# Performance work log

Hardware: AMD Instinct MI355X
Metric: run time of the kernel (lower is better)

## Reference

```python
import jax, jax.numpy as jnp
import numpy as np

B, N, F_IN = 64, 128, 128
H, MSG, L = 512, 512, 4
N_STEPS = 4
TARGET = 12
HIDDEN = (128, 256, 128)


def _mlp_params(key, n_in, n_out):
    dims = (n_in,) + HIDDEN + (n_out,)
    ps = []
    for i in range(len(dims) - 1):
        key, k1, k2 = jax.random.split(key, 3)
        s = 1.0 / np.sqrt(dims[i]).astype(np.float32)
        ps.append(jax.random.uniform(k1, (dims[i + 1], dims[i]), minval=-s, maxval=s, dtype=jnp.float32))
        ps.append(jax.random.uniform(k2, (dims[i + 1],), minval=-s, maxval=s, dtype=jnp.float32))
    return ps


def setup_inputs():
    key = jax.random.key(0)
    ks = jax.random.split(key, 10)
    g = (jax.random.uniform(ks[0], (B, N, N)) < 0.15).astype(jnp.float32)
    e = jax.random.randint(ks[1], (B, N, N), 0, L + 1).astype(jnp.float32) * g
    h_in = jax.random.normal(ks[2], (B, N, F_IN), dtype=jnp.float32)
    # trailing nodes are 'virtual' (zero features -> masked out by the model)
    node_on = (jnp.arange(N) < 112).astype(jnp.float32)
    h_in = h_in * node_on[None, :, None]
    g = g * node_on[None, :, None] * node_on[None, None, :]
    e = e * node_on[None, :, None] * node_on[None, None, :]
    A = jax.random.normal(ks[3], (L, H, MSG), dtype=jnp.float32)  # per-edge-label message matrices
    s = 1.0 / np.sqrt(H).astype(np.float32)
    gru_Wih = jax.random.uniform(ks[4], (3 * H, MSG), minval=-s, maxval=s, dtype=jnp.float32)
    gru_Whh = jax.random.uniform(ks[5], (3 * H, H), minval=-s, maxval=s, dtype=jnp.float32)
    gru_bih = jax.random.uniform(ks[6], (3 * H,), minval=-s, maxval=s, dtype=jnp.float32)
    gru_bhh = jax.random.uniform(ks[7], (3 * H,), minval=-s, maxval=s, dtype=jnp.float32)
    r1 = _mlp_params(ks[8], 2 * H, TARGET)
    r2 = _mlp_params(ks[9], H, TARGET)
    inp = dict(g=g, h_in=h_in, e=e, A=A, gru_Wih=gru_Wih, gru_Whh=gru_Whh,
               gru_bih=gru_bih, gru_bhh=gru_bhh)
    for i in range(4):
        inp['r1_W%d' % i], inp['r1_b%d' % i] = r1[2 * i], r1[2 * i + 1]
        inp['r2_W%d' % i], inp['r2_b%d' % i] = r2[2 * i], r2[2 * i + 1]
    return inp


def _mlp(x, Ws, bs):
    for W, b in zip(Ws[:-1], bs[:-1]):
        x = jax.nn.relu(x @ W.T + b)
    return x @ Ws[-1].T + bs[-1]


def _forward(g, h_in, e, A, gru_Wih, gru_Whh, gru_bih, gru_bhh, r1_Ws, r1_bs, r2_Ws, r2_bs):
    Bq, Nq, F = h_in.shape
    Lq, Hq, Mq = A.shape
    # zero-pad node features up to hidden size
    h0 = jnp.concatenate([h_in, jnp.zeros((Bq, Nq, Hq - F), h_in.dtype)], axis=-1)  # [B,N,H]
    node_mask = (jnp.sum(jnp.abs(h_in), axis=-1) > 0).astype(h_in.dtype)  # [B,N]
    labels = jnp.arange(1, Lq + 1, dtype=e.dtype)
    e_oh = (e[..., None] == labels).astype(h_in.dtype)  # [B,N,N,L] edge-label one-hot
    h = h0
    for _ in range(N_STEPS):
        # per-label projected states, then edge-conditioned masked-sum aggregation
        hproj = jnp.einsum('bwh,lhm->blwm', h, A)  # [B,L,N,MSG]
        m = jnp.einsum('bvwl,blwm,bvw->bvm', e_oh, hproj, g)  # [B,N,MSG]
        # one GRU step per node (vectorized), torch nn.GRU gate ordering r,z,n
        gi = m @ gru_Wih.T + gru_bih
        gh = h @ gru_Whh.T + gru_bhh
        i_r, i_z, i_n = jnp.split(gi, 3, axis=-1)
        h_r, h_z, h_n = jnp.split(gh, 3, axis=-1)
        r = jax.nn.sigmoid(i_r + h_r)
        z = jax.nn.sigmoid(i_z + h_z)
        n = jnp.tanh(i_n + r * h_n)
        h = ((1.0 - z) * n + z * h) * node_mask[..., None]
    # GGNN gated readout over nodes, masking virtual nodes
    gate = jax.nn.sigmoid(_mlp(jnp.concatenate([h, h0], axis=-1), r1_Ws, r1_bs))
    val = _mlp(h, r2_Ws, r2_bs)
    read_mask = (jnp.sum(h0, axis=-1) != 0).astype(h.dtype)  # [B,N]
    return jnp.sum(gate * val * read_mask[..., None], axis=1)  # [B,TARGET]


def reference(g, h_in, e, A, gru_Wih, gru_Whh, gru_bih, gru_bhh,
              r1_W0, r1_b0, r1_W1, r1_b1, r1_W2, r1_b2, r1_W3, r1_b3,
              r2_W0, r2_b0, r2_W1, r2_b1, r2_W2, r2_b2, r2_W3, r2_b3):
    return _forward(g, h_in, e, A, gru_Wih, gru_Whh, gru_bih, gru_bhh,
                    [r1_W0, r1_W1, r1_W2, r1_W3], [r1_b0, r1_b1, r1_b2, r1_b3],
                    [r2_W0, r2_W1, r2_W2, r2_W3], [r2_b0, r2_b1, r2_b2, r2_b3])
```

## Files before the change

### kernel.cpp

```cpp
#include <hip/hip_runtime.h>
#include <math.h>

#define B_     64
#define N_     128
#define FIN_   128
#define H_     512
#define MSG_   512
#define L_     4
#define NSTEPS_ 4
#define TGT_   12
#define ROWS_  (B_*N_)

typedef _Float16 f16;
typedef __attribute__((ext_vector_type(8))) _Float16 half8;
typedef __attribute__((ext_vector_type(4))) float f32x4;

__device__ inline void gload16(const void* g, void* l) {
    __builtin_amdgcn_global_load_lds((const __attribute__((address_space(1))) void*)g,
                                     (__attribute__((address_space(3))) void*)l,
                                     16, 0, 0);
}

__device__ inline void split_write(float v, f16* ph, f16* pl) {
    f16 hi = (f16)v;
    *ph = hi;
    *pl = (f16)(v - (float)hi);
}

__global__ void k_init(const float* __restrict__ h_in,
                       f16* __restrict__ hbh, f16* __restrict__ hbl,
                       float* __restrict__ nmask, float* __restrict__ rmask) {
    int bn = blockIdx.x;
    int t  = threadIdx.x;
    const float* src = h_in + (size_t)bn * FIN_;
    float v  = src[t];
    float sa = fabsf(v), ss = v;
    #pragma unroll
    for (int o = 32; o > 0; o >>= 1) {
        sa += __shfl_down(sa, o);
        ss += __shfl_down(ss, o);
    }
    __shared__ float wa[2], wsum[2];
    int wid = t >> 6, lane = t & 63;
    if (lane == 0) { wa[wid] = sa; wsum[wid] = ss; }
    __syncthreads();
    if (t == 0) {
        float ta = wa[0] + wa[1], ts = wsum[0] + wsum[1];
        nmask[bn] = (ta > 0.f) ? 1.f : 0.f;
        rmask[bn] = (ts != 0.f) ? 1.f : 0.f;
    }
    f16* bh = hbh + (size_t)bn * 1024;
    f16* bl = hbl + (size_t)bn * 1024;
    #pragma unroll
    for (int r = 0; r < 4; r++) {
        int j = t + r * 128;
        float val = (j < FIN_) ? src[j] : 0.f;
        f16 hi = (f16)val, lo = (f16)(val - (float)hi);
        bh[j] = hi; bl[j] = lo;
        bh[512 + j] = hi; bl[512 + j] = lo;
    }
}

__global__ void k_mkmask(const float* __restrict__ g, const float* __restrict__ e,
                         f16* __restrict__ Mm) {
    long idx = (long)blockIdx.x * 256 + threadIdx.x;
    if (idx >= (long)ROWS_ * 512) return;
    int w = idx & 127;
    int l = (idx >> 7) & 3;
    long bv = idx >> 9;
    float gv = g[bv * N_ + w];
    float ev = e[bv * N_ + w];
    Mm[idx] = (f16)((gv != 0.f && (int)ev == l + 1) ? 1.f : 0.f);
}

struct WSet {
    const float* s[10];
    f16* d[10];
    int nc[10];
    int ncp[10];
    int kk[10];
};
__global__ void k_convWs(WSet ws) {
    int ti = blockIdx.y;
    long idx = (long)blockIdx.x * 256 + threadIdx.x;
    int K = ws.kk[ti];
    long tot = (long)ws.ncp[ti] * K;
    if (idx >= tot) return;
    long n = idx / K;
    ws.d[ti][idx] = (f16)((n < ws.nc[ti]) ? ws.s[ti][idx] : 0.f);
}

__global__ void k_convA(const float* __restrict__ A, f16* __restrict__ ATh) {
    long idx = (long)blockIdx.x * 256 + threadIdx.x;
    long n = idx >> 11, k = idx & 2047;
    ATh[idx] = (f16)A[k * 512 + n];
}

__global__ __launch_bounds__(256, 4)
void k_proj(const f16* __restrict__ ATh, const f16* __restrict__ hb,
            f16* __restrict__ oh, f16* __restrict__ ol)
{
    __shared__ __align__(16) f16 As[2][4][128][8];
    __shared__ __align__(16) f16 Bs[2][4][128][8];
    const int tid = threadIdx.x;
    const int l = tid & 63, w = tid >> 6;
    const int wr = w >> 1, wc = w & 1;
    const int lz = blockIdx.z;
    const long m0 = (long)blockIdx.x * 128;
    const long n0 = (long)blockIdx.y * 128;

    f32x4 acc[4][4];
    #pragma unroll
    for (int i = 0; i < 4; i++)
        #pragma unroll
        for (int j = 0; j < 4; j++)
            acc[i][j] = (f32x4){0.f, 0.f, 0.f, 0.f};

    const int nt = 512 >> 5;

    auto stage = [&](int buf, int t) {
        long k0 = (long)t << 5;
        #pragma unroll
        for (int i = 0; i < 2; ++i) {
            int la = tid + i * 256;
            int row = la & 127, c = la >> 7;
            gload16(ATh + (m0 + row) * 2048 + lz * 512 + k0 + c * 8,
                    (f16*)As[buf] + (size_t)la * 8);
        }
        #pragma unroll
        for (int i = 0; i < 2; ++i) {
            int la = tid + i * 256;
            int col = la & 127, c = la >> 7;
            gload16(hb + (n0 + col) * 1024 + k0 + c * 8,
                    (f16*)Bs[buf] + (size_t)la * 8);
        }
    };

    stage(0, 0);
    for (int t = 0; t < nt; ++t) {
        int cur = t & 1;
        __syncthreads();
        if (t + 1 < nt) stage(cur ^ 1, t + 1);
        const int g = l >> 4, idx = l & 15;
        half8 bf[4];
        #pragma unroll
        for (int ct = 0; ct < 4; ++ct)
            bf[ct] = *(const half8*)&Bs[cur][g][wc * 64 + ct * 16 + idx][0];
        #pragma unroll
        for (int rt = 0; rt < 4; ++rt) {
            half8 ah = *(const half8*)&As[cur][g][wr * 64 + rt * 16 + idx][0];
            #pragma unroll
            for (int ct = 0; ct < 4; ++ct)
                acc[rt][ct] = __builtin_amdgcn_mfma_f32_16x16x32_f16(ah, bf[ct], acc[rt][ct], 0, 0, 0);
        }
    }

    #pragma unroll
    for (int rt = 0; rt < 4; ++rt)
        #pragma unroll
        for (int ct = 0; ct < 4; ++ct) {
            long col = n0 + wc * 64 + ct * 16 + (l & 15);
            long bb = col >> 7, ww = col & 127;
            #pragma unroll
            for (int j = 0; j < 4; ++j) {
                long row = m0 + wr * 64 + rt * 16 + (l >> 4) * 4 + j;
                size_t o = ((size_t)(bb * 512 + row)) * 512 + lz * 128 + ww;
                split_write(acc[rt][ct][j], oh + o, ol + o);
            }
        }
}

__global__ __launch_bounds__(256, 3)
void k_aggm(const f16* __restrict__ Mm, const f16* __restrict__ ph,
            const f16* __restrict__ pl_, f16* __restrict__ mh, f16* __restrict__ ml)
{
    __shared__ __align__(16) f16 As[2][4][128][8];
    __shared__ __align__(16) f16 Bs[2][2][4][128][8];
    const int tid = threadIdx.x;
    const int l = tid & 63, w = tid >> 6;
    const int wr = w >> 1, wc = w & 1;
    const long b  = blockIdx.y;
    const long n0 = (long)blockIdx.x * 128;
    const f16* Xb = Mm  + (size_t)b * 128 * 512;
    const f16* W0 = ph  + (size_t)b * 512 * 512;
    const f16* W1 = pl_ + (size_t)b * 512 * 512;

    f32x4 acc[4][4];
    #pragma unroll
    for (int i = 0; i < 4; i++)
        #pragma unroll
        for (int j = 0; j < 4; j++)
            acc[i][j] = (f32x4){0.f, 0.f, 0.f, 0.f};

    const int nt = 512 >> 5;

    auto stage = [&](int buf, int t) {
        long k0 = (long)t << 5;
        #pragma unroll
        for (int i = 0; i < 2; ++i) {
            int la = tid + i * 256;
            int row = la & 127, c = la >> 7;
            gload16(Xb + row * 512 + k0 + c * 8, (f16*)As[buf] + (size_t)la * 8);
        }
        #pragma unroll
        for (int i = 0; i < 4; ++i) {
            int la = tid + i * 256;
            int col = la & 127, c = (la >> 7) & 3, pl = la >> 9;
            gload16((pl ? W1 : W0) + (n0 + col) * 512 + k0 + c * 8,
                    (f16*)Bs[buf][pl] + (size_t)(la & 511) * 8);
        }
    };

    stage(0, 0);
    for (int t = 0; t < nt; ++t) {
        int cur = t & 1;
        __syncthreads();
        if (t + 1 < nt) stage(cur ^ 1, t + 1);
        const int g = l >> 4, idx = l & 15;
        half8 bfh[4], bfl[4];
        #pragma unroll
        for (int ct = 0; ct < 4; ++ct) {
            bfh[ct] = *(const half8*)&Bs[cur][0][g][wc * 64 + ct * 16 + idx][0];
            bfl[ct] = *(const half8*)&Bs[cur][1][g][wc * 64 + ct * 16 + idx][0];
        }
        #pragma unroll
        for (int rt = 0; rt < 4; ++rt) {
            half8 af = *(const half8*)&As[cur][g][wr * 64 + rt * 16 + idx][0];
            #pragma unroll
            for (int ct = 0; ct < 4; ++ct) {
                acc[rt][ct] = __builtin_amdgcn_mfma_f32_16x16x32_f16(af, bfh[ct], acc[rt][ct], 0, 0, 0);
                acc[rt][ct] = __builtin_amdgcn_mfma_f32_16x16x32_f16(af, bfl[ct], acc[rt][ct], 0, 0, 0);
            }
        }
    }

    #pragma unroll
    for (int rt = 0; rt < 4; ++rt)
        #pragma unroll
        for (int ct = 0; ct < 4; ++ct) {
            long col = n0 + wc * 64 + ct * 16 + (l & 15);
            #pragma unroll
            for (int j = 0; j < 4; ++j) {
                long row = wr * 64 + rt * 16 + (l >> 4) * 4 + j;
                size_t o = ((size_t)b * 128 + row) * 512 + col;
                split_write(acc[rt][ct][j], mh + o, ml + o);
            }
        }
}

__global__ __launch_bounds__(256, 2)
void k_gruG(const f16* __restrict__ mh, const f16* __restrict__ ml,
            const f16* __restrict__ Wih,
            const f16* __restrict__ hih, const f16* __restrict__ hil,
            const f16* __restrict__ Whh,
            const float* __restrict__ bih, const float* __restrict__ bhh,
            f16* __restrict__ hoh, f16* __restrict__ hol,
            const float* __restrict__ nmask)
{
    __shared__ __align__(16) f16 As[2][2][4][128][8];
    __shared__ __align__(16) f16 Bs[2][4][192][8];
    const int tid = threadIdx.x;
    const int l = tid & 63, w = tid >> 6;
    const int wr = w >> 1, wc = w & 1;
    const long m0 = (long)blockIdx.x * 128;
    const int  c0 = blockIdx.y * 64;

    f32x4 rz[2][4][2], ni[4][2], nh[4][2];
    #pragma unroll
    for (int rt = 0; rt < 4; ++rt)
        #pragma unroll
        for (int ct = 0; ct < 2; ++ct) {
            rz[0][rt][ct] = (f32x4){0.f, 0.f, 0.f, 0.f};
            rz[1][rt][ct] = (f32x4){0.f, 0.f, 0.f, 0.f};
            ni[rt][ct]    = (f32x4){0.f, 0.f, 0.f, 0.f};
            nh[rt][ct]    = (f32x4){0.f, 0.f, 0.f, 0.f};
        }

    auto stageB = [&](int buf, int t, const f16* W) {
        long k0 = (long)t << 5;
        #pragma unroll
        for (int i = 0; i < 3; ++i) {
            int la = tid + i * 256;
            int g = la / 192, cc = la - g * 192;
            int col = (cc >> 6) * 512 + c0 + (cc & 63);
            gload16(W + (size_t)col * 512 + k0 + g * 8,
                    (f16*)Bs[buf] + ((size_t)g * 192 + cc) * 8);
        }
    };
    auto stage1 = [&](int buf, int t) {
        long k0 = (long)t << 5;
        #pragma unroll
        for (int i = 0; i < 4; ++i) {
            int la = tid + i * 256;
            int pl = la >> 9, g = (la >> 7) & 3, row = la & 127;
            const f16* Xp = pl ? ml : mh;
            gload16(Xp + (m0 + row) * 512 + k0 + g * 8,
                    (f16*)As[buf][pl] + (size_t)(la & 511) * 8);
        }
        stageB(buf, t, Wih);
    };
    auto stage2 = [&](int buf, int t) {
        long k0 = (long)t << 5;
        #pragma unroll
        for (int i = 0; i < 2; ++i) {
            int la = tid + i * 256;
            int g = la >> 7, row = la & 127;
            gload16(hih + (m0 + row) * 1024 + k0 + g * 8,
                    (f16*)As[buf][0] + (size_t)la * 8);
        }
        stageB(buf, t, Whh);
    };

    const int g = l >> 4, idx = l & 15;

    stage1(0, 0);
    for (int t = 0; t < 16; ++t) {
        int cur = t & 1;
        __syncthreads();
        if (t + 1 < 16) stage1(cur ^ 1, t + 1);
        half8 bf[6];
        #pragma unroll
        for (int gc = 0; gc < 6; ++gc)
            bf[gc] = *(const half8*)&Bs[cur][g][(gc >> 1) * 64 + wc * 32 + (gc & 1) * 16 + idx][0];
        #pragma unroll
        for (int rt = 0; rt < 4; ++rt) {
            half8 ah = *(const half8*)&As[cur][0][g][wr * 64 + rt * 16 + idx][0];
            half8 al = *(const half8*)&As[cur][1][g][wr * 64 + rt * 16 + idx][0];
            #pragma unroll
            for (int ct = 0; ct < 2; ++ct) {
                rz[0][rt][ct] = __builtin_amdgcn_mfma_f32_16x16x32_f16(ah, bf[ct],     rz[0][rt][ct], 0, 0, 0);
                rz[0][rt][ct] = __builtin_amdgcn_mfma_f32_16x16x32_f16(al, bf[ct],     rz[0][rt][ct], 0, 0, 0);
                rz[1][rt][ct] = __builtin_amdgcn_mfma_f32_16x16x32_f16(ah, bf[2 + ct], rz[1][rt][ct], 0, 0, 0);
                rz[1][rt][ct] = __builtin_amdgcn_mfma_f32_16x16x32_f16(al, bf[2 + ct], rz[1][rt][ct], 0, 0, 0);
                ni[rt][ct]    = __builtin_amdgcn_mfma_f32_16x16x32_f16(ah, bf[4 + ct], ni[rt][ct],    0, 0, 0);
                ni[rt][ct]    = __builtin_amdgcn_mfma_f32_16x16x32_f16(al, bf[4 + ct], ni[rt][ct],    0, 0, 0);
            }
        }
    }

    stage2(0, 0);
    for (int t = 0; t < 16; ++t) {
        int cur = t & 1;
        __syncthreads();
        if (t + 1 < 16) stage2(cur ^ 1, t + 1);
        half8 bf[6];
        #pragma unroll
        for (int gc = 0; gc < 6; ++gc)
            bf[gc] = *(const half8*)&Bs[cur][g][(gc >> 1) * 64 + wc * 32 + (gc & 1) * 16 + idx][0];
        #pragma unroll
        for (int rt = 0; rt < 4; ++rt) {
            half8 ah = *(const half8*)&As[cur][0][g][wr * 64 + rt * 16 + idx][0];
            #pragma unroll
            for (int ct = 0; ct < 2; ++ct) {
                rz[0][rt][ct] = __builtin_amdgcn_mfma_f32_16x16x32_f16(ah, bf[ct],     rz[0][rt][ct], 0, 0, 0);
                rz[1][rt][ct] = __builtin_amdgcn_mfma_f32_16x16x32_f16(ah, bf[2 + ct], rz[1][rt][ct], 0, 0, 0);
                nh[rt][ct]    = __builtin_amdgcn_mfma_f32_16x16x32_f16(ah, bf[4 + ct], nh[rt][ct],    0, 0, 0);
            }
        }
    }

    #pragma unroll
    for (int rt = 0; rt < 4; ++rt)
        #pragma unroll
        for (int ct = 0; ct < 2; ++ct) {
            int c = c0 + wc * 32 + ct * 16 + idx;
            float br = bih[c]        + bhh[c];
            float bz = bih[512 + c]  + bhh[512 + c];
            float bni = bih[1024 + c];
            float bnh = bhh[1024 + c];
            #pragma unroll
            for (int j = 0; j < 4; ++j) {
                long row = m0 + wr * 64 + rt * 16 + g * 4 + j;
                float r = 1.f / (1.f + expf(-(rz[0][rt][ct][j] + br)));
                float z = 1.f / (1.f + expf(-(rz[1][rt][ct][j] + bz)));
                float n = tanhf(ni[rt][ct][j] + bni + r * (nh[rt][ct][j] + bnh));
                size_t o = (size_t)row * 1024 + c;
                float h_old = (float)hih[o] + (float)hil[o];
                float out = ((1.f - z) * n + z * h_old) * nmask[row];
                split_write(out, hoh + o, hol + o);
            }
        }
}

struct RP {
    const f16* X[2];  int ldx[2];
    const f16* W[2];  int ldw[2];
    const float* bias[2];
    float* Cf[2];  f16* Ch[2];
    int ldc[2];  int ncmax[2];  int K[2];
};
template<int OUT>
__global__ __launch_bounds__(256, 4)
void k_mfmaD(RP p) {
    const int z = blockIdx.z;
    const f16* Xh = p.X[z];  const int ldx = p.ldx[z];
    const f16* Wh = p.W[z];  const int ldw = p.ldw[z];
    const float* bias = p.bias[z];
    const int ldc = p.ldc[z], ncmax = p.ncmax[z], K = p.K[z];

    __shared__ __align__(16) f16 As[2][4][128][8];
    __shared__ __align__(16) f16 Bs[2][4][128][8];
    const int tid = threadIdx.x;
    const int l = tid & 63, w = tid >> 6;
    const int wr = w >> 1, wc = w & 1;
    const long m0 = (long)blockIdx.x * 128;
    const long n0 = (long)blockIdx.y * 128;

    f32x4 acc[4][4];
    #pragma unroll
    for (int i = 0; i < 4; i++)
        #pragma unroll
        for (int j = 0; j < 4; j++)
            acc[i][j] = (f32x4){0.f, 0.f, 0.f, 0.f};

    const int nt = K >> 5;

    auto stage = [&](int buf, int t) {
        long k0 = (long)t << 5;
        #pragma unroll
        for (int i = 0; i < 2; ++i) {
            int la = tid + i * 256;
            int row = la & 127, c = la >> 7;
            gload16(Xh + (m0 + row) * ldx + k0 + c * 8,
                    (f16*)As[buf] + (size_t)la * 8);
        }
        #pragma unroll
        for (int i = 0; i < 2; ++i) {
            int la = tid + i * 256;
            int col = la & 127, c = la >> 7;
            gload16(Wh + (n0 + col) * ldw + k0 + c * 8,
                    (f16*)Bs[buf] + (size_t)la * 8);
        }
    };

    stage(0, 0);
    for (int t = 0; t < nt; ++t) {
        int cur = t & 1;
        __syncthreads();
        if (t + 1 < nt) stage(cur ^ 1, t + 1);
        const int g = l >> 4, idx = l & 15;
        half8 bf[4];
        #pragma unroll
        for (int ct = 0; ct < 4; ++ct)
            bf[ct] = *(const half8*)&Bs[cur][g][wc * 64 + ct * 16 + idx][0];
        #pragma unroll
        for (int rt = 0; rt < 4; ++rt) {
            half8 ah = *(const half8*)&As[cur][g][wr * 64 + rt * 16 + idx][0];
            #pragma unroll
            for (int ct = 0; ct < 4; ++ct)
                acc[rt][ct] = __builtin_amdgcn_mfma_f32_16x16x32_f16(ah, bf[ct], acc[rt][ct], 0, 0, 0);
        }
    }

    #pragma unroll
    for (int rt = 0; rt < 4; ++rt)
        #pragma unroll
        for (int ct = 0; ct < 4; ++ct) {
            long col = n0 + wc * 64 + ct * 16 + (l & 15);
            if (col < ncmax) {
                float bv = bias ? bias[col] : 0.f;
                #pragma unroll
                for (int j = 0; j < 4; ++j) {
                    long row = m0 + wr * 64 + rt * 16 + (l >> 4) * 4 + j;
                    float v = acc[rt][ct][j] + bv;
                    if (OUT == 0) {
                        p.Cf[z][row * ldc + col] = v;
                    } else {
                        p.Ch[z][row * ldc + col] = (f16)fmaxf(v, 0.f);
                    }
                }
            }
        }
}

__global__ void k_readout(const float* __restrict__ gp, const float* __restrict__ vp,
                          const float* __restrict__ rmask, float* __restrict__ out) {
    int b = blockIdx.x;
    int t = threadIdx.x;
    float a[TGT_];
    const float* gr = gp + ((size_t)b * N_ + t) * TGT_;
    const float* vr = vp + ((size_t)b * N_ + t) * TGT_;
    float mk = rmask[b * N_ + t];
    #pragma unroll
    for (int j = 0; j < TGT_; j++)
        a[j] = (1.f / (1.f + expf(-gr[j]))) * vr[j] * mk;
    __shared__ float red[128][TGT_];
    #pragma unroll
    for (int j = 0; j < TGT_; j++) red[t][j] = a[j];
    __syncthreads();
    for (int off = 64; off > 0; off >>= 1) {
        if (t < off)
            #pragma unroll
            for (int j = 0; j < TGT_; j++) red[t][j] += red[t + off][j];
        __syncthreads();
    }
    if (t < TGT_) out[b * TGT_ + t] = red[0][t];
}

extern "C" void kernel_launch(void* const* d_in, const int* in_sizes, int n_in,
                              void* d_out, int out_size, void* d_ws, size_t ws_size,
                              hipStream_t stream) {
    const float* g    = (const float*)d_in[0];
    const float* h_in = (const float*)d_in[1];
    const float* e    = (const float*)d_in[2];
    const float* A    = (const float*)d_in[3];
    const float* Wih  = (const float*)d_in[4];
    const float* Whh  = (const float*)d_in[5];
    const float* bih  = (const float*)d_in[6];
    const float* bhh  = (const float*)d_in[7];

    const float *r1W[4], *r1b[4], *r2W[4], *r2b[4];
    bool interleaved = (in_sizes[10] == 128 * 512);
    if (interleaved) {
        for (int i = 0; i < 4; i++) {
            r1W[i] = (const float*)d_in[8 + 4 * i + 0];
            r1b[i] = (const float*)d_in[8 + 4 * i + 1];
            r2W[i] = (const float*)d_in[8 + 4 * i + 2];
            r2b[i] = (const float*)d_in[8 + 4 * i + 3];
        }
    } else {
        for (int i = 0; i < 4; i++) {
            r1W[i] = (const float*)d_in[8 + 2 * i + 0];
            r1b[i] = (const float*)d_in[8 + 2 * i + 1];
            r2W[i] = (const float*)d_in[16 + 2 * i + 0];
            r2b[i] = (const float*)d_in[16 + 2 * i + 1];
        }
    }

    char* ws = (char*)d_ws;
    size_t off = 0;
    auto alloc = [&](size_t bytes) { char* p = ws + off; off += bytes; return p; };

    f16* hbh[2]; f16* hbl[2];
    hbh[0] = (f16*)alloc((size_t)ROWS_ * 1024 * 2);
    hbl[0] = (f16*)alloc((size_t)ROWS_ * 1024 * 2);
    hbh[1] = (f16*)alloc((size_t)ROWS_ * 1024 * 2);
    hbl[1] = (f16*)alloc((size_t)ROWS_ * 1024 * 2);
    f16* mh = (f16*)alloc((size_t)ROWS_ * 512 * 2);
    f16* ml = (f16*)alloc((size_t)ROWS_ * 512 * 2);
    f16* Mm = (f16*)alloc((size_t)ROWS_ * 512 * 2);
    char* hat = alloc((size_t)2 * 4 * 512 * 8192 * 2);
    f16*  hATh = (f16*)hat;
    f16*  hATl = (f16*)(hat + (size_t)4 * 512 * 8192 * 2);
    f16*   ta1 = (f16*)hat;
    f16*   tb1 = ta1 + (size_t)ROWS_ * 128;
    f16*   ta2 = tb1 + (size_t)ROWS_ * 256;
    f16*   tb2 = ta2 + (size_t)ROWS_ * 128;
    float* gp  = (float*)(tb2 + (size_t)ROWS_ * 256);
    float* vp  = gp + (size_t)ROWS_ * TGT_;
    f16* ATh  = (f16*)alloc((size_t)512 * 2048 * 2);
    f16* Wihh = (f16*)alloc((size_t)1536 * 512 * 2);
    f16* Whhh = (f16*)alloc((size_t)1536 * 512 * 2);
    f16* rWh[8];
    const int rNc[8]  = {128, 256, 128, TGT_, 128, 256, 128, TGT_};
    const int rNcp[8] = {128, 256, 128, 128,  128, 256, 128, 128};
    const int rK[8]   = {1024, 128, 256, 128, 512, 128, 256, 128};
    for (int i = 0; i < 8; i++)
        rWh[i] = (f16*)alloc((size_t)rNcp[i] * rK[i] * 2);
    float* nm = (float*)alloc(ROWS_ * 4);
    float* rm = (float*)alloc(ROWS_ * 4);
    (void)ws_size;

    k_convA<<<(512 * 2048) / 256, 256, 0, stream>>>(A, ATh);
    {
        WSet wset;
        const float* srcs[10] = {Wih, Whh, r1W[0], r1W[1], r1W[2], r1W[3],
                                 r2W[0], r2W[1], r2W[2], r2W[3]};
        f16* dsts[10] = {Wihh, Whhh, rWh[0], rWh[1], rWh[2], rWh[3],
                         rWh[4], rWh[5], rWh[6], rWh[7]};
        int ncs[10]  = {1536, 1536, rNc[0], rNc[1], rNc[2], rNc[3], rNc[4], rNc[5], rNc[6], rNc[7]};
        int ncps[10] = {1536, 1536, rNcp[0], rNcp[1], rNcp[2], rNcp[3], rNcp[4], rNcp[5], rNcp[6], rNcp[7]};
        int ks[10]   = {512, 512, rK[0], rK[1], rK[2], rK[3], rK[4], rK[5], rK[6], rK[7]};
        for (int i = 0; i < 10; i++) {
            wset.s[i] = srcs[i]; wset.d[i] = dsts[i];
            wset.nc[i] = ncs[i]; wset.ncp[i] = ncps[i]; wset.kk[i] = ks[i];
        }
        int maxblocks = (1536 * 512 + 255) / 256;
        k_convWs<<<dim3(maxblocks, 10), 256, 0, stream>>>(wset);
    }
    k_mkmask<<<((long)ROWS_ * 512 + 255) / 256, 256, 0, stream>>>(g, e, Mm);
    k_init<<<ROWS_, 128, 0, stream>>>(h_in, hbh[0], hbl[0], nm, rm);

    for (int step = 0; step < NSTEPS_; step++) {
        int cur = step & 1, nxt = cur ^ 1;
        k_proj<<<dim3(4, 64, 4), 256, 0, stream>>>(ATh, hbh[cur], hATh, hATl);
        k_aggm<<<dim3(4, 64), 256, 0, stream>>>(Mm, hATh, hATl, mh, ml);
        k_gruG<<<dim3(64, 8), 256, 0, stream>>>(mh, ml, Wihh, hbh[cur], hbl[cur],
                                                Whhh, bih, bhh, hbh[nxt], hbl[nxt], nm);
    }

    auto setRP = [&](RP& p, int zi, const f16* X, int ldx, const f16* W, int ldw,
                     const float* bias, float* Cf, f16* Ch, int ldc, int ncmax, int K) {
        p.X[zi] = X; p.ldx[zi] = ldx; p.W[zi] = W; p.ldw[zi] = ldw;
        p.bias[zi] = bias; p.Cf[zi] = Cf; p.Ch[zi] = Ch;
        p.ldc[zi] = ldc; p.ncmax[zi] = ncmax; p.K[zi] = K;
    };
    RP p0, p1, p2, p3;
    setRP(p0, 0, hbh[0], 1024, rWh[0], 1024, r1b[0], nullptr, ta1, 128, 128, 1024);
    setRP(p0, 1, hbh[0], 1024, rWh[4],  512, r2b[0], nullptr, ta2, 128, 128,  512);
    setRP(p1, 0, ta1, 128, rWh[1], 128, r1b[1], nullptr, tb1, 256, 256, 128);
    setRP(p1, 1, ta2, 128, rWh[5], 128, r2b[1], nullptr, tb2, 256, 256, 128);
    setRP(p2, 0, tb1, 256, rWh[2], 256, r1b[2], nullptr, ta1, 128, 128, 256);
    setRP(p2, 1, tb2, 256, rWh[6], 256, r2b[2], nullptr, ta2, 128, 128, 256);
    setRP(p3, 0, ta1, 128, rWh[3], 128, r1b[3], gp, nullptr, TGT_, TGT_, 128);
    setRP(p3, 1, ta2, 128, rWh[7], 128, r2b[3], vp, nullptr, TGT_, TGT_, 128);
    k_mfmaD<1><<<dim3(64, 1, 2), 256, 0, stream>>>(p0);
    k_mfmaD<1><<<dim3(64, 2, 2), 256, 0, stream>>>(p1);
    k_mfmaD<1><<<dim3(64, 1, 2), 256, 0, stream>>>(p2);
    k_mfmaD<0><<<dim3(64, 1, 2), 256, 0, stream>>>(p3);

    k_readout<<<B_, 128, 0, stream>>>(gp, vp, rm, (float*)d_out);
}
```

Measured before the change: 805.0 us.

## Drop hi/lo fp16 split for projected and aggregated messages

Removes the two-term fp16 (hi+lo) representation of the per-label projections and aggregated messages, storing single fp16 values instead. This halves the buffer traffic and MFMA count in the aggregation and GRU input-gate GEMMs and shrinks shared memory, which allows raising launch bounds occupancy for k_aggm and k_gruG. The cost is lower numerical precision of intermediate messages, which may affect accuracy against the fp32 reference.

```diff
diff --git a/kernel.cpp b/kernel.cpp
--- a/kernel.cpp
+++ b/kernel.cpp
@@ -98,7 +98,7 @@
 
 __global__ __launch_bounds__(256, 4)
 void k_proj(const f16* __restrict__ ATh, const f16* __restrict__ hb,
-            f16* __restrict__ oh, f16* __restrict__ ol)
+            f16* __restrict__ oh)
 {
     __shared__ __align__(16) f16 As[2][4][128][8];
     __shared__ __align__(16) f16 Bs[2][4][128][8];
@@ -165,25 +165,24 @@
             for (int j = 0; j < 4; ++j) {
                 long row = m0 + wr * 64 + rt * 16 + (l >> 4) * 4 + j;
                 size_t o = ((size_t)(bb * 512 + row)) * 512 + lz * 128 + ww;
-                split_write(acc[rt][ct][j], oh + o, ol + o);
+                oh[o] = (f16)acc[rt][ct][j];
             }
         }
 }
 
-__global__ __launch_bounds__(256, 3)
+__global__ __launch_bounds__(256, 4)
 void k_aggm(const f16* __restrict__ Mm, const f16* __restrict__ ph,
-            const f16* __restrict__ pl_, f16* __restrict__ mh, f16* __restrict__ ml)
+            f16* __restrict__ mh)
 {
     __shared__ __align__(16) f16 As[2][4][128][8];
-    __shared__ __align__(16) f16 Bs[2][2][4][128][8];
+    __shared__ __align__(16) f16 Bs[2][4][128][8];
     const int tid = threadIdx.x;
     const int l = tid & 63, w = tid >> 6;
     const int wr = w >> 1, wc = w & 1;
     const long b  = blockIdx.y;
     const long n0 = (long)blockIdx.x * 128;
-    const f16* Xb = Mm  + (size_t)b * 128 * 512;
-    const f16* W0 = ph  + (size_t)b * 512 * 512;
-    const f16* W1 = pl_ + (size_t)b * 512 * 512;
+    const f16* Xb = Mm + (size_t)b * 128 * 512;
+    const f16* W0 = ph + (size_t)b * 512 * 512;
 
     f32x4 acc[4][4];
     #pragma unroll
@@ -203,11 +202,11 @@
             gload16(Xb + row * 512 + k0 + c * 8, (f16*)As[buf] + (size_t)la * 8);
         }
         #pragma unroll
-        for (int i = 0; i < 4; ++i) {
-            int la = tid + i * 256;
-            int col = la & 127, c = (la >> 7) & 3, pl = la >> 9;
-            gload16((pl ? W1 : W0) + (n0 + col) * 512 + k0 + c * 8,
-                    (f16*)Bs[buf][pl] + (size_t)(la & 511) * 8);
+        for (int i = 0; i < 2; ++i) {
+            int la = tid + i * 256;
+            int col = la & 127, c = la >> 7;
+            gload16(W0 + (n0 + col) * 512 + k0 + c * 8,
+                    (f16*)Bs[buf] + (size_t)la * 8);
         }
     };
 
@@ -217,20 +216,16 @@
         __syncthreads();
         if (t + 1 < nt) stage(cur ^ 1, t + 1);
         const int g = l >> 4, idx = l & 15;
-        half8 bfh[4], bfl[4];
-        #pragma unroll
-        for (int ct = 0; ct < 4; ++ct) {
-            bfh[ct] = *(const half8*)&Bs[cur][0][g][wc * 64 + ct * 16 + idx][0];
-            bfl[ct] = *(const half8*)&Bs[cur][1][g][wc * 64 + ct * 16 + idx][0];
-        }
+        half8 bf[4];
+        #pragma unroll
+        for (int ct = 0; ct < 4; ++ct)
+            bf[ct] = *(const half8*)&Bs[cur][g][wc * 64 + ct * 16 + idx][0];
         #pragma unroll
         for (int rt = 0; rt < 4; ++rt) {
             half8 af = *(const half8*)&As[cur][g][wr * 64 + rt * 16 + idx][0];
             #pragma unroll
-            for (int ct = 0; ct < 4; ++ct) {
-                acc[rt][ct] = __builtin_amdgcn_mfma_f32_16x16x32_f16(af, bfh[ct], acc[rt][ct], 0, 0, 0);
-                acc[rt][ct] = __builtin_amdgcn_mfma_f32_16x16x32_f16(af, bfl[ct], acc[rt][ct], 0, 0, 0);
-            }
+            for (int ct = 0; ct < 4; ++ct)
+                acc[rt][ct] = __builtin_amdgcn_mfma_f32_16x16x32_f16(af, bf[ct], acc[rt][ct], 0, 0, 0);
         }
     }
 
@@ -243,13 +238,13 @@
             for (int j = 0; j < 4; ++j) {
                 long row = wr * 64 + rt * 16 + (l >> 4) * 4 + j;
                 size_t o = ((size_t)b * 128 + row) * 512 + col;
-                split_write(acc[rt][ct][j], mh + o, ml + o);
+                mh[o] = (f16)acc[rt][ct][j];
             }
         }
 }
 
-__global__ __launch_bounds__(256, 2)
-void k_gruG(const f16* __restrict__ mh, const f16* __restrict__ ml,
+__global__ __launch_bounds__(256, 4)
+void k_gruG(const f16* __restrict__ mh,
             const f16* __restrict__ Wih,
             const f16* __restrict__ hih, const f16* __restrict__ hil,
             const f16* __restrict__ Whh,
@@ -257,7 +252,7 @@
             f16* __restrict__ hoh, f16* __restrict__ hol,
             const float* __restrict__ nmask)
 {
-    __shared__ __align__(16) f16 As[2][2][4][128][8];
+    __shared__ __align__(16) f16 As[2][4][128][8];
     __shared__ __align__(16) f16 Bs[2][4][192][8];
     const int tid = threadIdx.x;
     const int l = tid & 63, w = tid >> 6;
@@ -287,69 +282,53 @@
                     (f16*)Bs[buf] + ((size_t)g * 192 + cc) * 8);
         }
     };
-    auto stage1 = [&](int buf, int t) {
+    auto stageA = [&](int buf, int t, const f16* X, int ldx) {
         long k0 = (long)t << 5;
         #pragma unroll
-        for (int i = 0; i < 4; ++i) {
-            int la = tid + i * 256;
-            int pl = la >> 9, g = (la >> 7) & 3, row = la & 127;
-            const f16* Xp = pl ? ml : mh;
-            gload16(Xp + (m0 + row) * 512 + k0 + g * 8,
-                    (f16*)As[buf][pl] + (size_t)(la & 511) * 8);
-        }
-        stageB(buf, t, Wih);
+        for (int i = 0; i < 2; ++i) {
+            int la = tid + i * 256;
+            int g = la >> 7, row = la & 127;
+            gload16(X + (size_t)(m0 + row) * ldx + k0 + g * 8,
+                    (f16*)As[buf] + (size_t)la * 8);
+        }
     };
-    auto stage2 = [&](int buf, int t) {
-        long k0 = (long)t << 5;
-        #pragma unroll
-        for (int i = 0; i < 2; ++i) {
-            int la = tid + i * 256;
-            int g = la >> 7, row = la & 127;
-            gload16(hih + (m0 + row) * 1024 + k0 + g * 8,
-                    (f16*)As[buf][0] + (size_t)la * 8);
-        }
-        stageB(buf, t, Whh);
-    };
 
     const int g = l >> 4, idx = l & 15;
 
-    stage1(0, 0);
+    stageA(0, 0, mh, 512); stageB(0, 0, Wih);
     for (int t = 0; t < 16; ++t) {
         int cur = t & 1;
         __syncthreads();
-        if (t + 1 < 16) stage1(cur ^ 1, t + 1);
+        if (t + 1 < 16) { stageA(cur ^ 1, t + 1, mh, 512); stageB(cur ^ 1, t + 1, Wih); }
         half8 bf[6];
         #pragma unroll
         for (int gc = 0; gc < 6; ++gc)
             bf[gc] = *(const half8*)&Bs[cur][g][(gc >> 1) * 64 + wc * 32 + (gc & 1) * 16 + idx][0];
         #pragma unroll
         for (int rt = 0; rt < 4; ++rt) {
-            half8 ah = *(const half8*)&As[cur][0][g][wr * 64 + rt * 16 + idx][0];
-            half8 al = *(const half8*)&As[cur][1][g][wr * 64 + rt * 16 + idx][0];
+            half8 ah = *(const half8*)&As[cur][g][wr * 64 + rt * 16 + idx][0];
             #pragma unroll
             for (int ct = 0; ct < 2; ++ct) {
                 rz[0][rt][ct] = __builtin_amdgcn_mfma_f32_16x16x32_f16(ah, bf[ct],     rz[0][rt][ct], 0, 0, 0);
-                rz[0][rt][ct] = __builtin_amdgcn_mfma_f32_16x16x32_f16(al, bf[ct],     rz[0][rt][ct], 0, 0, 0);
                 rz[1][rt][ct] = __builtin_amdgcn_mfma_f32_16x16x32_f16(ah, bf[2 + ct], rz[1][rt][ct], 0, 0, 0);
-                rz[1][rt][ct] = __builtin_amdgcn_mfma_f32_16x16x32_f16(al, bf[2 + ct], rz[1][rt][ct], 0, 0, 0);
                 ni[rt][ct]    = __builtin_amdgcn_mfma_f32_16x16x32_f16(ah, bf[4 + ct], ni[rt][ct],    0, 0, 0);
-                ni[rt][ct]    = __builtin_amdgcn_mfma_f32_16x16x32_f16(al, bf[4 + ct], ni[rt][ct],    0, 0, 0);
             }
         }
     }
-
-    stage2(0, 0);
+    __syncthreads();
+
+    stageA(0, 0, hih, 1024); stageB(0, 0, Whh);
     for (int t = 0; t < 16; ++t) {
         int cur = t & 1;
         __syncthreads();
-        if (t + 1 < 16) stage2(cur ^ 1, t + 1);
+        if (t + 1 < 16) { stageA(cur ^ 1, t + 1, hih, 1024); stageB(cur ^ 1, t + 1, Whh); }
         half8 bf[6];
         #pragma unroll
         for (int gc = 0; gc < 6; ++gc)
             bf[gc] = *(const half8*)&Bs[cur][g][(gc >> 1) * 64 + wc * 32 + (gc & 1) * 16 + idx][0];
         #pragma unroll
         for (int rt = 0; rt < 4; ++rt) {
-            half8 ah = *(const half8*)&As[cur][0][g][wr * 64 + rt * 16 + idx][0];
+            half8 ah = *(const half8*)&As[cur][g][wr * 64 + rt * 16 + idx][0];
             #pragma unroll
             for (int ct = 0; ct < 2; ++ct) {
                 rz[0][rt][ct] = __builtin_amdgcn_mfma_f32_16x16x32_f16(ah, bf[ct],     rz[0][rt][ct], 0, 0, 0);
@@ -537,11 +516,9 @@
     hbh[1] = (f16*)alloc((size_t)ROWS_ * 1024 * 2);
     hbl[1] = (f16*)alloc((size_t)ROWS_ * 1024 * 2);
     f16* mh = (f16*)alloc((size_t)ROWS_ * 512 * 2);
-    f16* ml = (f16*)alloc((size_t)ROWS_ * 512 * 2);
     f16* Mm = (f16*)alloc((size_t)ROWS_ * 512 * 2);
-    char* hat = alloc((size_t)2 * 4 * 512 * 8192 * 2);
+    char* hat = alloc((size_t)4 * 512 * 8192 * 2);
     f16*  hATh = (f16*)hat;
-    f16*  hATl = (f16*)(hat + (size_t)4 * 512 * 8192 * 2);
     f16*   ta1 = (f16*)hat;
     f16*   tb1 = ta1 + (size_t)ROWS_ * 128;
     f16*   ta2 = tb1 + (size_t)ROWS_ * 256;
@@ -583,9 +560,9 @@
 
     for (int step = 0; step < NSTEPS_; step++) {
         int cur = step & 1, nxt = cur ^ 1;
-        k_proj<<<dim3(4, 64, 4), 256, 0, stream>>>(ATh, hbh[cur], hATh, hATl);
-        k_aggm<<<dim3(4, 64), 256, 0, stream>>>(Mm, hATh, hATl, mh, ml);
-        k_gruG<<<dim3(64, 8), 256, 0, stream>>>(mh, ml, Wihh, hbh[cur], hbl[cur],
+        k_proj<<<dim3(4, 64, 4), 256, 0, stream>>>(ATh, hbh[cur], hATh);
+        k_aggm<<<dim3(4, 64), 256, 0, stream>>>(Mm, hATh, mh);
+        k_gruG<<<dim3(64, 8), 256, 0, stream>>>(mh, Wihh, hbh[cur], hbl[cur],
                                                 Whhh, bih, bhh, hbh[nxt], hbl[nxt], nm);
     }
 
```

After: 947.2 us. +17.7%, slower.
